# Optimization experiments

Measured on AMD Instinct MI355X. Metric: run time of the kernel, lower is better.

Reference implementation:

```python
import jax, jax.numpy as jnp
import numpy as np

D_MODEL = 1024
NUM_HEADS = 16
HEAD_DIM = D_MODEL // NUM_HEADS
D_FF = 4096
LN_EPS = 1e-6  # flax nnx.LayerNorm default


def setup_inputs() -> dict:
    key = jax.random.key(0)
    ks = jax.random.split(key, 13)
    s_in = 1.0 / np.sqrt(D_MODEL)
    s_ff = 1.0 / np.sqrt(D_FF)
    return {
        "x": jax.random.normal(ks[0], (2, 2048, D_MODEL), dtype=jnp.float32),
        "Wq": jax.random.normal(ks[1], (D_MODEL, D_MODEL), jnp.float32) * s_in,
        "bq": jnp.zeros((D_MODEL,), jnp.float32),
        "Wk": jax.random.normal(ks[2], (D_MODEL, D_MODEL), jnp.float32) * s_in,
        "bk": jnp.zeros((D_MODEL,), jnp.float32),
        "Wv": jax.random.normal(ks[3], (D_MODEL, D_MODEL), jnp.float32) * s_in,
        "bv": jnp.zeros((D_MODEL,), jnp.float32),
        "Wo": jax.random.normal(ks[4], (D_MODEL, D_MODEL), jnp.float32) * s_in,
        "bo": jnp.zeros((D_MODEL,), jnp.float32),
        "W1": jax.random.normal(ks[5], (D_MODEL, D_FF), jnp.float32) * s_in,
        "b1": jnp.zeros((D_FF,), jnp.float32),
        "W2": jax.random.normal(ks[6], (D_FF, D_MODEL), jnp.float32) * s_ff,
        "b2": jnp.zeros((D_MODEL,), jnp.float32),
        "ln1_scale": jnp.ones((D_MODEL,), jnp.float32),
        "ln1_bias": jnp.zeros((D_MODEL,), jnp.float32),
        "ln2_scale": jnp.ones((D_MODEL,), jnp.float32),
        "ln2_bias": jnp.zeros((D_MODEL,), jnp.float32),
    }


def layer_norm(x, scale, bias):
    mu = jnp.mean(x, axis=-1, keepdims=True)
    var = jnp.mean(jnp.square(x - mu), axis=-1, keepdims=True)
    return (x - mu) * jax.lax.rsqrt(var + LN_EPS) * scale + bias


def reference(x, Wq, bq, Wk, bk, Wv, bv, Wo, bo, W1, b1, W2, b2,
              ln1_scale, ln1_bias, ln2_scale, ln2_bias):
    B, S, _ = x.shape
    h = layer_norm(x, ln1_scale, ln1_bias)
    # project and split heads: [B, H, S, Dh]
    q = (h @ Wq + bq).reshape(B, S, NUM_HEADS, HEAD_DIM).transpose(0, 2, 1, 3)
    k = (h @ Wk + bk).reshape(B, S, NUM_HEADS, HEAD_DIM).transpose(0, 2, 1, 3)
    v = (h @ Wv + bv).reshape(B, S, NUM_HEADS, HEAD_DIM).transpose(0, 2, 1, 3)
    scores = jnp.einsum("bhqd,bhkd->bhqk", q, k) / jnp.sqrt(jnp.float32(HEAD_DIM))
    attn = jax.nn.softmax(scores, axis=-1)
    out = jnp.einsum("bhqk,bhkd->bhqd", attn, v)
    out = out.transpose(0, 2, 1, 3).reshape(B, S, D_MODEL)
    x = x + out @ Wo + bo
    h2 = layer_norm(x, ln2_scale, ln2_bias)
    ff = jax.nn.relu(h2 @ W1 + b1) @ W2 + b2
    return x + ff
```

## Files before the change

kernel.cpp:

```cpp
#include <hip/hip_runtime.h>

typedef unsigned short ushort_t;
typedef __attribute__((ext_vector_type(8))) __bf16 bf16x8;
typedef __attribute__((ext_vector_type(8))) unsigned short ushort8v;
typedef __attribute__((ext_vector_type(4))) float floatx4;

__device__ inline float b2f(ushort_t u) {
    union { unsigned int i; float f; } c; c.i = ((unsigned int)u) << 16; return c.f;
}
__device__ inline ushort_t f2b(float f) {
    union { float f; unsigned int i; } c; c.f = f;
    unsigned int i = c.i;
    unsigned int r = (i + 0x7FFFu + ((i >> 16) & 1u)) >> 16;
    return (ushort_t)r;
}
__device__ inline bf16x8 as_bf16x8(ushort8v u) { return __builtin_bit_cast(bf16x8, u); }

__device__ inline void load_lds16(const ushort_t* g, ushort_t* l) {
    __builtin_amdgcn_global_load_lds(
        (const __attribute__((address_space(1))) void*)g,
        (__attribute__((address_space(3))) void*)l, 16, 0, 0);
}

__global__ __launch_bounds__(256) void concat3_kernel(
    const float* __restrict__ a, const float* __restrict__ b,
    const float* __restrict__ c, float* __restrict__ o) {
    int t = blockIdx.x * 256 + threadIdx.x;
    if (t < 3072)
        o[t] = t < 1024 ? a[t] : (t < 2048 ? b[t - 1024] : c[t - 2048]);
}

__global__ __launch_bounds__(256) void copy_f32_kernel(
    const float* __restrict__ src, float* __restrict__ dst) {
    size_t i = ((size_t)blockIdx.x * 256 + threadIdx.x) * 4;
    *(float4*)(dst + i) = *(const float4*)(src + i);
}

__global__ __launch_bounds__(256) void transpose_all_kernel(
    const float* __restrict__ Wq, const float* __restrict__ Wk,
    const float* __restrict__ Wv, const float* __restrict__ Wo,
    const float* __restrict__ W1, const float* __restrict__ W2,
    ushort_t* __restrict__ dq, ushort_t* __restrict__ dk,
    ushort_t* __restrict__ dv, ushort_t* __restrict__ do_,
    ushort_t* __restrict__ d1, ushort_t* __restrict__ d2) {
    int t = blockIdx.x;
    const float* src; ushort_t* dst; int R, ld, tcx, tcy;
    if (t < 4096) {
        int id = t >> 10, u = t & 1023;
        tcx = u & 31; tcy = u >> 5; R = 1024; ld = 1024;
        src = id == 0 ? Wq : id == 1 ? Wk : id == 2 ? Wv : Wo;
        dst = id == 0 ? dq : id == 1 ? dk : id == 2 ? dv : do_;
    } else if (t < 8192) {
        int u = t - 4096;
        tcx = u & 127; tcy = u >> 7; R = 1024; ld = 4096;
        src = W1; dst = d1;
    } else {
        int u = t - 8192;
        tcx = u & 31; tcy = u >> 5; R = 4096; ld = 1024;
        src = W2; dst = d2;
    }
    __shared__ float tile[32][33];
    int tx = threadIdx.x, ty = threadIdx.y;
    int r0 = tcy * 32, c0 = tcx * 32;
#pragma unroll
    for (int i = 0; i < 32; i += 8)
        tile[ty + i][tx] = src[(size_t)(r0 + ty + i) * ld + c0 + tx];
    __syncthreads();
#pragma unroll
    for (int i = 0; i < 32; i += 8)
        dst[(size_t)(c0 + ty + i) * R + r0 + tx] = f2b(tile[tx][ty + i]);
}

__global__ __launch_bounds__(256) void transpose_v_kernel(
    const ushort_t* __restrict__ qkv, ushort_t* __restrict__ vt) {
    __shared__ ushort_t tile[32][33];
    int tx = threadIdx.x, ty = threadIdx.y;
    int s0 = blockIdx.x * 32, d0 = blockIdx.y * 32;
    int bh = blockIdx.z, b = bh >> 4, h = bh & 15;
    const ushort_t* src = qkv + (size_t)b * 2048 * 3072 + 2048 + h * 64;
    ushort_t* dst = vt + (size_t)bh * 64 * 2048;
#pragma unroll
    for (int i = 0; i < 32; i += 8)
        tile[ty + i][tx] = src[(size_t)(s0 + ty + i) * 3072 + d0 + tx];
    __syncthreads();
#pragma unroll
    for (int i = 0; i < 32; i += 8)
        dst[(size_t)(d0 + ty + i) * 2048 + s0 + tx] = tile[tx][ty + i];
}

__device__ inline float wave_sum(float s) {
#pragma unroll
    for (int o = 32; o > 0; o >>= 1) s += __shfl_xor(s, o);
    return s;
}

__global__ __launch_bounds__(256) void ln_f32_kernel(
    const float* __restrict__ x, const float* __restrict__ sc,
    const float* __restrict__ bi, ushort_t* __restrict__ out) {
    int row = blockIdx.x, t = threadIdx.x;
    const float* xr = x + (size_t)row * 1024;
    float4 u = *(const float4*)(xr + t * 4);
    float v0 = u.x, v1 = u.y, v2 = u.z, v3 = u.w;
    __shared__ float sm[8];
    int wv = t >> 6, lane = t & 63;
    float s = wave_sum(v0 + v1 + v2 + v3);
    if (lane == 0) sm[wv] = s;
    __syncthreads();
    float mean = (sm[0] + sm[1] + sm[2] + sm[3]) * (1.0f / 1024.0f);
    float d0 = v0 - mean, d1 = v1 - mean, d2 = v2 - mean, d3 = v3 - mean;
    float q = wave_sum(d0 * d0 + d1 * d1 + d2 * d2 + d3 * d3);
    if (lane == 0) sm[4 + wv] = q;
    __syncthreads();
    float var = (sm[4] + sm[5] + sm[6] + sm[7]) * (1.0f / 1024.0f);
    float rn = rsqrtf(var + 1e-6f);
    float4 us = *(const float4*)(sc + t * 4);
    float4 ub = *(const float4*)(bi + t * 4);
    ushort4 o;
    o.x = f2b(d0 * rn * us.x + ub.x);
    o.y = f2b(d1 * rn * us.y + ub.y);
    o.z = f2b(d2 * rn * us.z + ub.z);
    o.w = f2b(d3 * rn * us.w + ub.w);
    *(ushort4*)(out + (size_t)row * 1024 + t * 4) = o;
}

__global__ __launch_bounds__(256) void gemm_bt_kernel(
    const ushort_t* __restrict__ A, const ushort_t* __restrict__ Bt,
    const float* __restrict__ bias, const float* __restrict__ resf,
    ushort_t* __restrict__ Cb, float* __restrict__ Cf,
    int M, int N, int K, int ldb, int op) {
    __shared__ __align__(16) ushort_t As[128 * 64];
    __shared__ __align__(16) ushort_t Bs[128 * 64];
    int tid = threadIdx.x;
    int m0 = blockIdx.y * 128, n0 = blockIdx.x * 128;
    int wv = tid >> 6, lane = tid & 63;
    int wr = wv & 1, wc = wv >> 1;
    int mo = wr * 64, no = wc * 64;
    int quad = lane >> 4, l16 = lane & 15;
    int k8 = quad * 8;

    floatx4 acc[4][4] = {};

    for (int k0 = 0; k0 < K; k0 += 64) {
#pragma unroll
        for (int c = 0; c < 4; ++c) {
            int e = c * 2048 + tid * 8;
            int r = e >> 6, kk = e & 63;
            int wbase = c * 2048 + wv * 512;
            load_lds16(A + (size_t)(m0 + r) * K + k0 + kk, As + wbase);
            load_lds16(Bt + (size_t)(n0 + r) * ldb + k0 + kk, Bs + wbase);
        }
        __syncthreads();
#pragma unroll
        for (int h = 0; h < 2; ++h) {
            bf16x8 af[4], bfr[4];
#pragma unroll
            for (int i = 0; i < 4; ++i) {
                af[i]  = as_bf16x8(*(const ushort8v*)(As + (mo + i * 16 + l16) * 64 + h * 32 + k8));
                bfr[i] = as_bf16x8(*(const ushort8v*)(Bs + (no + i * 16 + l16) * 64 + h * 32 + k8));
            }
#pragma unroll
            for (int mi = 0; mi < 4; ++mi)
#pragma unroll
                for (int ni = 0; ni < 4; ++ni)
                    acc[mi][ni] = __builtin_amdgcn_mfma_f32_16x16x32_bf16(
                        af[mi], bfr[ni], acc[mi][ni], 0, 0, 0);
        }
        __syncthreads();
    }

#pragma unroll
    for (int mi = 0; mi < 4; ++mi) {
#pragma unroll
        for (int r = 0; r < 4; ++r) {
            int row = m0 + mo + mi * 16 + quad * 4 + r;
            size_t rowoff = (size_t)row * N;
#pragma unroll
            for (int ni = 0; ni < 4; ++ni) {
                int col = n0 + no + ni * 16 + l16;
                float val = acc[mi][ni][r];
                if (op != 3) val += bias[col];
                if (op == 1) val = fmaxf(val, 0.0f);
                if (op >= 2) {
                    val += resf[rowoff + col];
                    Cf[rowoff + col] = val;
                } else {
                    Cb[rowoff + col] = f2b(val);
                }
            }
        }
    }
}

__global__ __launch_bounds__(256) void gemm_bt_atomic_kernel(
    const ushort_t* __restrict__ A, const ushort_t* __restrict__ Bt,
    const float* __restrict__ bias, float* __restrict__ Cf,
    int M, int N, int lda, int ldb, int Kc) {
    __shared__ __align__(16) ushort_t As[128 * 64];
    __shared__ __align__(16) ushort_t Bs[128 * 64];
    int tid = threadIdx.x;
    int m0 = blockIdx.y * 128, n0 = blockIdx.x * 128;
    int kbase = blockIdx.z * Kc;
    int wv = tid >> 6, lane = tid & 63;
    int wr = wv & 1, wc = wv >> 1;
    int mo = wr * 64, no = wc * 64;
    int quad = lane >> 4, l16 = lane & 15;
    int k8 = quad * 8;

    floatx4 acc[4][4] = {};

    for (int k0 = kbase; k0 < kbase + Kc; k0 += 64) {
#pragma unroll
        for (int c = 0; c < 4; ++c) {
            int e = c * 2048 + tid * 8;
            int r = e >> 6, kk = e & 63;
            int wbase = c * 2048 + wv * 512;
            load_lds16(A + (size_t)(m0 + r) * lda + k0 + kk, As + wbase);
            load_lds16(Bt + (size_t)(n0 + r) * ldb + k0 + kk, Bs + wbase);
        }
        __syncthreads();
#pragma unroll
        for (int h = 0; h < 2; ++h) {
            bf16x8 af[4], bfr[4];
#pragma unroll
            for (int i = 0; i < 4; ++i) {
                af[i]  = as_bf16x8(*(const ushort8v*)(As + (mo + i * 16 + l16) * 64 + h * 32 + k8));
                bfr[i] = as_bf16x8(*(const ushort8v*)(Bs + (no + i * 16 + l16) * 64 + h * 32 + k8));
            }
#pragma unroll
            for (int mi = 0; mi < 4; ++mi)
#pragma unroll
                for (int ni = 0; ni < 4; ++ni)
                    acc[mi][ni] = __builtin_amdgcn_mfma_f32_16x16x32_bf16(
                        af[mi], bfr[ni], acc[mi][ni], 0, 0, 0);
        }
        __syncthreads();
    }

    bool addb = (blockIdx.z == 0) && (bias != nullptr);
#pragma unroll
    for (int mi = 0; mi < 4; ++mi) {
#pragma unroll
        for (int r = 0; r < 4; ++r) {
            int row = m0 + mo + mi * 16 + quad * 4 + r;
            size_t rowoff = (size_t)row * N;
#pragma unroll
            for (int ni = 0; ni < 4; ++ni) {
                int col = n0 + no + ni * 16 + l16;
                float val = acc[mi][ni][r];
                if (addb) val += bias[col];
                unsafeAtomicAdd(&Cf[rowoff + col], val);
            }
        }
    }
}

__global__ __launch_bounds__(256) void attn_kernel(
    const ushort_t* __restrict__ qkv, const ushort_t* __restrict__ vt,
    ushort_t* __restrict__ om) {
    const int LDQ = 3072, LDO = 1024;
    int bh = blockIdx.y;
    int b = bh >> 4, h = bh & 15;
    size_t qbase = (size_t)b * 2048 * LDQ + h * 64;
    size_t kbase = qbase + 1024;
    const ushort_t* vtp = vt + (size_t)bh * 64 * 2048;
    int q0 = blockIdx.x * 128;
    int tid = threadIdx.x, wv = tid >> 6, lane = tid & 63;
    int quad = lane >> 4, l16 = lane & 15;
    int k8 = quad * 8;

    __shared__ __align__(16) ushort_t Ks[64 * 72];
    __shared__ __align__(16) ushort_t Vs[64 * 72];
    __shared__ __align__(16) ushort_t Ps[4 * 32 * 76];
    ushort_t* ps = Ps + wv * 32 * 76;

    int sr0 = tid >> 3, scc0 = (tid & 7) * 8;
    int sr1 = sr0 + 32;

    bf16x8 qf[2][2];
#pragma unroll
    for (int mt = 0; mt < 2; ++mt) {
        const ushort_t* qptr = qkv + qbase + (size_t)(q0 + wv * 32 + mt * 16 + l16) * LDQ;
        qf[mt][0] = as_bf16x8(*(const ushort8v*)(qptr + k8));
        qf[mt][1] = as_bf16x8(*(const ushort8v*)(qptr + 32 + k8));
    }

    bf16x8 ones;
#pragma unroll
    for (int j = 0; j < 8; ++j) ones[j] = (__bf16)1.0f;

    floatx4 Oacc[2][4] = {};
    floatx4 lsum[2] = {};

    ushort8v kreg0, kreg1, vreg0, vreg1;
    kreg0 = *(const ushort8v*)(qkv + kbase + (size_t)sr0 * LDQ + scc0);
    kreg1 = *(const ushort8v*)(qkv + kbase + (size_t)sr1 * LDQ + scc0);
    vreg0 = *(const ushort8v*)(vtp + (size_t)sr0 * 2048 + scc0);
    vreg1 = *(const ushort8v*)(vtp + (size_t)sr1 * 2048 + scc0);

    for (int kb = 0; kb < 2048; kb += 64) {
        __syncthreads();
        *(ushort8v*)(Ks + sr0 * 72 + scc0) = kreg0;
        *(ushort8v*)(Ks + sr1 * 72 + scc0) = kreg1;
        *(ushort8v*)(Vs + sr0 * 72 + scc0) = vreg0;
        *(ushort8v*)(Vs + sr1 * 72 + scc0) = vreg1;
        __syncthreads();

        int nkb = (kb + 64 < 2048) ? kb + 64 : 0;
        kreg0 = *(const ushort8v*)(qkv + kbase + (size_t)(nkb + sr0) * LDQ + scc0);
        kreg1 = *(const ushort8v*)(qkv + kbase + (size_t)(nkb + sr1) * LDQ + scc0);
        vreg0 = *(const ushort8v*)(vtp + (size_t)sr0 * 2048 + nkb + scc0);
        vreg1 = *(const ushort8v*)(vtp + (size_t)sr1 * 2048 + nkb + scc0);

        bf16x8 kf[4][2];
#pragma unroll
        for (int kt = 0; kt < 4; ++kt)
#pragma unroll
            for (int ds = 0; ds < 2; ++ds)
                kf[kt][ds] = as_bf16x8(
                    *(const ushort8v*)(Ks + (kt * 16 + l16) * 72 + ds * 32 + k8));

        floatx4 sc[2][4];
#pragma unroll
        for (int mt = 0; mt < 2; ++mt)
#pragma unroll
            for (int kt = 0; kt < 4; ++kt) {
                floatx4 s = {0.0f, 0.0f, 0.0f, 0.0f};
                s = __builtin_amdgcn_mfma_f32_16x16x32_bf16(qf[mt][0], kf[kt][0], s, 0, 0, 0);
                s = __builtin_amdgcn_mfma_f32_16x16x32_bf16(qf[mt][1], kf[kt][1], s, 0, 0, 0);
                sc[mt][kt] = s;
            }

#pragma unroll
        for (int mt = 0; mt < 2; ++mt)
#pragma unroll
            for (int kt = 0; kt < 4; ++kt)
#pragma unroll
                for (int r = 0; r < 4; ++r)
                    ps[(mt * 16 + quad * 4 + r) * 76 + kt * 16 + l16] =
                        f2b(__expf(sc[mt][kt][r] * 0.125f));

        bf16x8 vf[4][2];
#pragma unroll
        for (int dt = 0; dt < 4; ++dt)
#pragma unroll
            for (int ks = 0; ks < 2; ++ks)
                vf[dt][ks] = as_bf16x8(
                    *(const ushort8v*)(Vs + (dt * 16 + l16) * 72 + ks * 32 + k8));
#pragma unroll
        for (int mt = 0; mt < 2; ++mt) {
            bf16x8 pf0 = as_bf16x8(*(const ushort8v*)(ps + (mt * 16 + l16) * 76 + k8));
            bf16x8 pf1 = as_bf16x8(*(const ushort8v*)(ps + (mt * 16 + l16) * 76 + 32 + k8));
#pragma unroll
            for (int dt = 0; dt < 4; ++dt) {
                Oacc[mt][dt] = __builtin_amdgcn_mfma_f32_16x16x32_bf16(pf0, vf[dt][0], Oacc[mt][dt], 0, 0, 0);
                Oacc[mt][dt] = __builtin_amdgcn_mfma_f32_16x16x32_bf16(pf1, vf[dt][1], Oacc[mt][dt], 0, 0, 0);
            }
            lsum[mt] = __builtin_amdgcn_mfma_f32_16x16x32_bf16(pf0, ones, lsum[mt], 0, 0, 0);
            lsum[mt] = __builtin_amdgcn_mfma_f32_16x16x32_bf16(pf1, ones, lsum[mt], 0, 0, 0);
        }
    }

#pragma unroll
    for (int mt = 0; mt < 2; ++mt)
#pragma unroll
        for (int r = 0; r < 4; ++r) {
            float inv = 1.0f / lsum[mt][r];
            size_t rowoff = (size_t)(b * 2048 + q0 + wv * 32 + mt * 16 + quad * 4 + r) * LDO + h * 64;
#pragma unroll
            for (int dt = 0; dt < 4; ++dt)
                om[rowoff + dt * 16 + l16] = f2b(Oacc[mt][dt][r] * inv);
        }
}

extern "C" void kernel_launch(void* const* d_in, const int* in_sizes, int n_in,
                              void* d_out, int out_size, void* d_ws, size_t ws_size,
                              hipStream_t stream) {
    const float* x    = (const float*)d_in[0];
    const float* Wq   = (const float*)d_in[1];
    const float* bq   = (const float*)d_in[2];
    const float* Wk   = (const float*)d_in[3];
    const float* bk   = (const float*)d_in[4];
    const float* Wv   = (const float*)d_in[5];
    const float* bv   = (const float*)d_in[6];
    const float* Wo   = (const float*)d_in[7];
    const float* bo   = (const float*)d_in[8];
    const float* W1   = (const float*)d_in[9];
    const float* b1   = (const float*)d_in[10];
    const float* W2   = (const float*)d_in[11];
    const float* b2   = (const float*)d_in[12];
    const float* ln1s = (const float*)d_in[13];
    const float* ln1b = (const float*)d_in[14];
    const float* ln2s = (const float*)d_in[15];
    const float* ln2b = (const float*)d_in[16];
    float*    outf = (float*)d_out;
    ushort_t* ws   = (ushort_t*)d_ws;

    const size_t M1 = 1048576;
    ushort_t* qkvT    = ws;
    ushort_t* WoT     = ws + 3 * M1;
    ushort_t* W1T     = ws + 4 * M1;
    ushort_t* W2T     = ws + 8 * M1;
    ushort_t* h       = ws + 12 * M1;
    ushort_t* attnout = ws + 12 * M1;
    ushort_t* qkv     = ws + 16 * M1;
    ushort_t* h2      = ws;
    ushort_t* ffbuf   = ws + 12 * M1;
    float*    bqkv    = (float*)d_out;
    ushort_t* vtbuf   = (ushort_t*)d_out;

    dim3 tb(32, 8);

    concat3_kernel<<<12, 256, 0, stream>>>(bq, bk, bv, bqkv);
    transpose_all_kernel<<<12288, tb, 0, stream>>>(
        Wq, Wk, Wv, Wo, W1, W2,
        qkvT, qkvT + M1, qkvT + 2 * M1, WoT, W1T, W2T);

    ln_f32_kernel<<<4096, 256, 0, stream>>>(x, ln1s, ln1b, h);

    gemm_bt_kernel<<<dim3(24, 32), 256, 0, stream>>>(
        h, qkvT, bqkv, nullptr, qkv, nullptr, 4096, 3072, 1024, 1024, 0);

    transpose_v_kernel<<<dim3(64, 2, 32), tb, 0, stream>>>(qkv, vtbuf);

    attn_kernel<<<dim3(16, 32), 256, 0, stream>>>(qkv, vtbuf, attnout);

    copy_f32_kernel<<<4096, 256, 0, stream>>>(x, outf);
    gemm_bt_atomic_kernel<<<dim3(8, 32, 4), 256, 0, stream>>>(
        attnout, WoT, bo, outf, 4096, 1024, 1024, 1024, 256);

    ln_f32_kernel<<<4096, 256, 0, stream>>>(outf, ln2s, ln2b, h2);

    gemm_bt_kernel<<<dim3(32, 32), 256, 0, stream>>>(
        h2, W1T, b1, nullptr, ffbuf, nullptr, 4096, 4096, 1024, 1024, 1);

    gemm_bt_atomic_kernel<<<dim3(8, 32, 2), 256, 0, stream>>>(
        ffbuf, W2T, b2, outf, 4096, 1024, 4096, 4096, 2048);
}
```

Baseline: 520.8 us.

## Load K/V fragments directly from global in attention, use native bf16 convert, deepen W2 split-K

The attention kernel drops its shared-memory staging of K and V tiles, along with both per-iteration __syncthreads. Each wave now loads its K and V MFMA fragments straight from global memory, relying on L1/L2 since all four waves read the same tile. The probability conversion switches from a manual rounding routine to the native __bf16 cast. Separately, the W2 atomic GEMM goes from split-K of 2 to 4, giving more blocks at the cost of more atomic adds. The direct loads lose the register prefetch that previously overlapped global latency with compute and quadruple global/L1 traffic per block.

```diff
diff --git a/kernel.cpp b/kernel.cpp
--- a/kernel.cpp
+++ b/kernel.cpp
@@ -261,20 +261,15 @@
     int bh = blockIdx.y;
     int b = bh >> 4, h = bh & 15;
     size_t qbase = (size_t)b * 2048 * LDQ + h * 64;
-    size_t kbase = qbase + 1024;
+    const ushort_t* kp = qkv + qbase + 1024;
     const ushort_t* vtp = vt + (size_t)bh * 64 * 2048;
     int q0 = blockIdx.x * 128;
     int tid = threadIdx.x, wv = tid >> 6, lane = tid & 63;
     int quad = lane >> 4, l16 = lane & 15;
     int k8 = quad * 8;
 
-    __shared__ __align__(16) ushort_t Ks[64 * 72];
-    __shared__ __align__(16) ushort_t Vs[64 * 72];
     __shared__ __align__(16) ushort_t Ps[4 * 32 * 76];
     ushort_t* ps = Ps + wv * 32 * 76;
-
-    int sr0 = tid >> 3, scc0 = (tid & 7) * 8;
-    int sr1 = sr0 + 32;
 
     bf16x8 qf[2][2];
 #pragma unroll
@@ -291,33 +286,14 @@
     floatx4 Oacc[2][4] = {};
     floatx4 lsum[2] = {};
 
-    ushort8v kreg0, kreg1, vreg0, vreg1;
-    kreg0 = *(const ushort8v*)(qkv + kbase + (size_t)sr0 * LDQ + scc0);
-    kreg1 = *(const ushort8v*)(qkv + kbase + (size_t)sr1 * LDQ + scc0);
-    vreg0 = *(const ushort8v*)(vtp + (size_t)sr0 * 2048 + scc0);
-    vreg1 = *(const ushort8v*)(vtp + (size_t)sr1 * 2048 + scc0);
-
     for (int kb = 0; kb < 2048; kb += 64) {
-        __syncthreads();
-        *(ushort8v*)(Ks + sr0 * 72 + scc0) = kreg0;
-        *(ushort8v*)(Ks + sr1 * 72 + scc0) = kreg1;
-        *(ushort8v*)(Vs + sr0 * 72 + scc0) = vreg0;
-        *(ushort8v*)(Vs + sr1 * 72 + scc0) = vreg1;
-        __syncthreads();
-
-        int nkb = (kb + 64 < 2048) ? kb + 64 : 0;
-        kreg0 = *(const ushort8v*)(qkv + kbase + (size_t)(nkb + sr0) * LDQ + scc0);
-        kreg1 = *(const ushort8v*)(qkv + kbase + (size_t)(nkb + sr1) * LDQ + scc0);
-        vreg0 = *(const ushort8v*)(vtp + (size_t)sr0 * 2048 + nkb + scc0);
-        vreg1 = *(const ushort8v*)(vtp + (size_t)sr1 * 2048 + nkb + scc0);
-
         bf16x8 kf[4][2];
 #pragma unroll
-        for (int kt = 0; kt < 4; ++kt)
-#pragma unroll
-            for (int ds = 0; ds < 2; ++ds)
-                kf[kt][ds] = as_bf16x8(
-                    *(const ushort8v*)(Ks + (kt * 16 + l16) * 72 + ds * 32 + k8));
+        for (int kt = 0; kt < 4; ++kt) {
+            const ushort_t* kr = kp + (size_t)(kb + kt * 16 + l16) * LDQ + k8;
+            kf[kt][0] = as_bf16x8(*(const ushort8v*)(kr));
+            kf[kt][1] = as_bf16x8(*(const ushort8v*)(kr + 32));
+        }
 
         floatx4 sc[2][4];
 #pragma unroll
@@ -335,17 +311,20 @@
 #pragma unroll
             for (int kt = 0; kt < 4; ++kt)
 #pragma unroll
-                for (int r = 0; r < 4; ++r)
+                for (int r = 0; r < 4; ++r) {
+                    __bf16 pb = (__bf16)__expf(sc[mt][kt][r] * 0.125f);
                     ps[(mt * 16 + quad * 4 + r) * 76 + kt * 16 + l16] =
-                        f2b(__expf(sc[mt][kt][r] * 0.125f));
+                        __builtin_bit_cast(ushort_t, pb);
+                }
 
         bf16x8 vf[4][2];
 #pragma unroll
-        for (int dt = 0; dt < 4; ++dt)
-#pragma unroll
-            for (int ks = 0; ks < 2; ++ks)
-                vf[dt][ks] = as_bf16x8(
-                    *(const ushort8v*)(Vs + (dt * 16 + l16) * 72 + ks * 32 + k8));
+        for (int dt = 0; dt < 4; ++dt) {
+            const ushort_t* vr = vtp + (size_t)(dt * 16 + l16) * 2048 + kb + k8;
+            vf[dt][0] = as_bf16x8(*(const ushort8v*)(vr));
+            vf[dt][1] = as_bf16x8(*(const ushort8v*)(vr + 32));
+        }
+
 #pragma unroll
         for (int mt = 0; mt < 2; ++mt) {
             bf16x8 pf0 = as_bf16x8(*(const ushort8v*)(ps + (mt * 16 + l16) * 76 + k8));
@@ -433,6 +412,6 @@
     gemm_bt_kernel<<<dim3(32, 32), 256, 0, stream>>>(
         h2, W1T, b1, nullptr, ffbuf, nullptr, 4096, 4096, 1024, 1024, 1);
 
-    gemm_bt_atomic_kernel<<<dim3(8, 32, 2), 256, 0, stream>>>(
-        ffbuf, W2T, b2, outf, 4096, 1024, 4096, 4096, 2048);
-}
+    gemm_bt_atomic_kernel<<<dim3(8, 32, 4), 256, 0, stream>>>(
+        ffbuf, W2T, b2, outf, 4096, 1024, 4096, 4096, 1024);
+}
```

Result: slower. 571.3 us (+9.7%).
